# Performance work log

Measured on AMD Instinct MI355X. Metric: run time of the kernel, lower is better.

The kernel has to match this reference:

```python
import jax, jax.numpy as jnp
import numpy as np

N_NODES, N_EDGES, D, H = 100000, 640000, 128, 128


def setup_inputs() -> dict:
    key = jax.random.key(0)
    k = jax.random.split(key, 5)
    x = jax.random.normal(k[0], (N_NODES, D), dtype=jnp.float32)
    edge_idx = jax.random.randint(k[1], (2, N_EDGES), 0, N_NODES)
    eps = jnp.zeros((1,), dtype=jnp.float32)  # nn.Parameter(torch.zeros(1))
    # MLP params: Linear(D,H) -> ReLU -> Linear(H,D)
    W1 = jax.random.normal(k[2], (D, H), dtype=jnp.float32) / np.sqrt(D).astype(np.float32)
    b1 = jnp.zeros((H,), dtype=jnp.float32)
    W2 = jax.random.normal(k[3], (H, D), dtype=jnp.float32) / np.sqrt(H).astype(np.float32)
    b2 = jnp.zeros((D,), dtype=jnp.float32)
    return dict(x=x, edge_idx=edge_idx, eps=eps, W1=W1, b1=b1, W2=W2, b2=b2)


def reference(x, edge_idx, eps, W1, b1, W2, b2):
    # gather src node features, scatter-add into dst rows
    src, dst = edge_idx[0], edge_idx[1]
    agg = jax.ops.segment_sum(x[src], dst, num_segments=x.shape[0])  # [N, D]
    out = (1.0 + eps) * x + agg  # eps-weighted residual
    h = jax.nn.relu(out @ W1 + b1)
    return h @ W2 + b2
```

## Files before the change

kernel.cpp:

```cpp
#include <hip/hip_runtime.h>

#define DD 128
typedef unsigned int uint;
typedef unsigned short ushort;

typedef __attribute__((ext_vector_type(8))) __bf16 bf16x8;
typedef __attribute__((ext_vector_type(8))) short short8;
typedef __attribute__((ext_vector_type(4))) float f32x4;

__device__ inline short f2bf_bits(float f) {
  union { float f; unsigned u; } x; x.f = f;
  unsigned r = x.u + 0x7fffu + ((x.u >> 16) & 1u);
  return (short)(r >> 16);
}
__device__ inline float bflo(uint u) { return __uint_as_float(u << 16); }
__device__ inline float bfhi(uint u) { return __uint_as_float(u & 0xffff0000u); }

__global__ void k_zero(int* __restrict__ p, int n) {
  int i = blockIdx.x * blockDim.x + threadIdx.x;
  if (i < n) p[i] = 0;
}

#define CHUNK 2048
__global__ __launch_bounds__(256) void k_bin(const int* __restrict__ ei, int ne,
                                             int* __restrict__ scur, uint* __restrict__ pairs32,
                                             const float4* __restrict__ xf4,
                                             short8* __restrict__ xb8, int nx8,
                                             const float* __restrict__ W1,
                                             const float* __restrict__ W2,
                                             ushort* __restrict__ wbf, int nbins) {
  __shared__ uint st[CHUNK];
  __shared__ ushort stb[CHUNK];
  __shared__ int hist[512];
  __shared__ int sc[512];
  __shared__ int loff[512];
  __shared__ int cur[512];
  __shared__ int gb[512];

  const int tid = threadIdx.x;
  const int sb = blockIdx.x & 63;
  const long base = (long)blockIdx.x * CHUNK;
  int m = (int)(ne - base);
  if (m > CHUNK) m = CHUNK;
  if (m < 0) m = 0;

  const int i0 = tid, i1 = tid + 256;
  hist[i0] = 0; hist[i1] = 0;
  cur[i0] = 0;  cur[i1] = 0;
  __syncthreads();

  uint wreg[8];
  int breg[8];
#pragma unroll
  for (int i = 0; i < 8; ++i) {
    int idx = i * 256 + tid;
    if (idx < m) {
      uint s = (uint)ei[base + idx];
      uint d = (uint)ei[(long)ne + base + idx];
      breg[i] = (int)(d >> 8);
      wreg[i] = (s << 8) | (d & 255u);
      atomicAdd(&hist[breg[i]], 1);
    } else {
      breg[i] = -1;
    }
  }
  __syncthreads();

  sc[i0] = hist[i0]; sc[i1] = hist[i1];
  __syncthreads();
  for (int d = 1; d < 512; d <<= 1) {
    int t0 = (i0 >= d) ? sc[i0 - d] : 0;
    int t1 = (i1 >= d) ? sc[i1 - d] : 0;
    __syncthreads();
    sc[i0] += t0; sc[i1] += t1;
    __syncthreads();
  }
  loff[i0] = sc[i0] - hist[i0];
  loff[i1] = sc[i1] - hist[i1];
  if (i0 < nbins && hist[i0] > 0) gb[i0] = atomicAdd(&scur[i0 * 64 + sb], hist[i0]);
  if (i1 < nbins && hist[i1] > 0) gb[i1] = atomicAdd(&scur[i1 * 64 + sb], hist[i1]);
  __syncthreads();

#pragma unroll
  for (int i = 0; i < 8; ++i) {
    if (breg[i] >= 0) {
      int p = atomicAdd(&cur[breg[i]], 1);
      int pos = loff[breg[i]] + p;
      st[pos] = wreg[i];
      stb[pos] = (ushort)breg[i];
    }
  }
  __syncthreads();

  for (int i = tid; i < m; i += 256) {
    int b = stb[i];
    int k = i - loff[b];
    int g = gb[b] + k;
    if (g < 128)
      pairs32[(long)b * 16384 + (sb << 8) + g] = st[i];
  }

  int t = blockIdx.x * 256 + tid;
  int stride = gridDim.x * 256;
  for (int c = t; c < nx8; c += stride) {
    float4 a = xf4[2 * c], b = xf4[2 * c + 1];
    short8 o;
    o[0] = f2bf_bits(a.x); o[1] = f2bf_bits(a.y); o[2] = f2bf_bits(a.z); o[3] = f2bf_bits(a.w);
    o[4] = f2bf_bits(b.x); o[5] = f2bf_bits(b.y); o[6] = f2bf_bits(b.z); o[7] = f2bf_bits(b.w);
    xb8[c] = o;
  }
  if (t < 16384) {
    int k = t >> 7, n = t & 127;
    wbf[128 * n + 8 * ((k >> 3) ^ (n & 7)) + (k & 7)] = (ushort)f2bf_bits(W1[t]);
  } else if (t < 32768) {
    int e = t - 16384;
    int k = e >> 7, n = e & 127;
    wbf[16384 + 128 * n + 8 * ((k >> 3) ^ (n & 7)) + (k & 7)] = (ushort)f2bf_bits(W2[e]);
  }
}

#define SUBCAP 128
__global__ __launch_bounds__(256) void k_bucket(const uint* __restrict__ pairs32,
                                                const int* __restrict__ scur,
                                                int* __restrict__ slot,
                                                int* __restrict__ cnt, int n) {
  __shared__ uint st[64 * SUBCAP];
  __shared__ int cs[64];
  __shared__ int cur[256];
  const int b = blockIdx.x;
  const int tid = threadIdx.x;
  if (tid < 64) {
    int c = scur[b * 64 + tid];
    cs[tid] = c < SUBCAP ? c : SUBCAP;
  }
  cur[tid] = 0;
  __syncthreads();
  for (int k = tid; k < 64 * SUBCAP; k += 256) {
    int s = k >> 7, i = k & (SUBCAP - 1);
    if (i < cs[s]) st[k] = pairs32[(long)b * 16384 + (s << 8) + i];
  }
  __syncthreads();
  for (int k = tid; k < 64 * SUBCAP; k += 256) {
    int s = k >> 7, i = k & (SUBCAP - 1);
    if (i < cs[s]) {
      uint w = st[k];
      int d = (int)(w & 255u);
      int p = atomicAdd(&cur[d], 1);
      if (p < 64) slot[(long)b * 16384 + d * 64 + p] = (int)(w >> 8);
    }
  }
  __syncthreads();
  int node = (b << 8) + tid;
  if (node < n) cnt[node] = cur[tid];
}

__global__ __launch_bounds__(256) void k_agg2(const uint* __restrict__ xb,
                                              const float* __restrict__ eps,
                                              const int* __restrict__ cnt,
                                              const int* __restrict__ slot,
                                              uint* __restrict__ agb, int n) {
  int wv = (blockIdx.x * 256 + threadIdx.x) >> 6;
  int lane = threadIdx.x & 63;
  int r0 = wv * 2, r1 = r0 + 1;
  if (r0 >= n) return;
  bool has1 = (r1 < n);
  float s = 1.0f + eps[0];

  uint u0 = xb[(long)r0 * 64 + lane];
  float a0x = s * bflo(u0), a0y = s * bfhi(u0);
  int d0 = cnt[r0];
  int m0 = d0 < 64 ? d0 : 64;
  int src0 = (lane < m0) ? slot[(long)r0 * 64 + lane] : 0;

  float a1x = 0.0f, a1y = 0.0f;
  int m1 = 0, src1 = 0;
  if (has1) {
    uint u1 = xb[(long)r1 * 64 + lane];
    a1x = s * bflo(u1); a1y = s * bfhi(u1);
    int d1 = cnt[r1];
    m1 = d1 < 64 ? d1 : 64;
    src1 = (lane < m1) ? slot[(long)r1 * 64 + lane] : 0;
  }

  int mm = m0 > m1 ? m0 : m1;
  for (int j = 0; j < mm; j += 4) {
    uint v0[4], v1[4];
#pragma unroll
    for (int k = 0; k < 4; ++k) {
      if (j + k < m0) { int ss = __shfl(src0, j + k); v0[k] = xb[(long)ss * 64 + lane]; }
      if (j + k < m1) { int ss = __shfl(src1, j + k); v1[k] = xb[(long)ss * 64 + lane]; }
    }
#pragma unroll
    for (int k = 0; k < 4; ++k) {
      if (j + k < m0) { a0x += bflo(v0[k]); a0y += bfhi(v0[k]); }
      if (j + k < m1) { a1x += bflo(v1[k]); a1y += bfhi(v1[k]); }
    }
  }

  uint o0 = ((uint)(ushort)f2bf_bits(a0y) << 16) | (uint)(ushort)f2bf_bits(a0x);
  agb[(long)r0 * 64 + lane] = o0;
  if (has1) {
    uint o1 = ((uint)(ushort)f2bf_bits(a1y) << 16) | (uint)(ushort)f2bf_bits(a1x);
    agb[(long)r1 * 64 + lane] = o1;
  }
}

__global__ __launch_bounds__(256) void k_mlp_bf(const ushort* __restrict__ agb,
                                                const ushort* __restrict__ wbf,
                                                const float* __restrict__ b1,
                                                const float* __restrict__ b2,
                                                float* __restrict__ out, int nrows) {
  __shared__ __align__(16) short Wt[2 * 16384];
  __shared__ __align__(16) short Hb[4][16 * 128];

  const int tid = threadIdx.x;
  const int lane = tid & 63;
  const int w = tid >> 6;
  const int l15 = lane & 15;
  const int g = lane >> 4;
  const int brow = blockIdx.x * 128;

  {
    const short8* ws8 = (const short8*)wbf;
    short8* wd8 = (short8*)Wt;
#pragma unroll
    for (int it = 0; it < 16; ++it) wd8[it * 256 + tid] = ws8[it * 256 + tid];
  }

  union U8 { short8 s; bf16x8 b; };

  U8 afr[2][4];
#pragma unroll
  for (int h = 0; h < 2; ++h) {
    int arow = brow + 64 * h + 16 * w + l15;
    if (arow < nrows) {
      const short8* ap = reinterpret_cast<const short8*>(agb + (long)arow * DD);
#pragma unroll
      for (int s = 0; s < 4; ++s) afr[h][s].s = ap[4 * s + g];
    } else {
#pragma unroll
      for (int s = 0; s < 4; ++s) {
        short8 t;
#pragma unroll
        for (int jj = 0; jj < 8; ++jj) t[jj] = 0;
        afr[h][s].s = t;
      }
    }
  }

  __syncthreads();

#pragma unroll
  for (int h = 0; h < 2; ++h) {
    const int wrow = brow + 64 * h + 16 * w;

    f32x4 acc[8];
#pragma unroll
    for (int nf = 0; nf < 8; ++nf) acc[nf] = (f32x4)(0.0f);
#pragma unroll
    for (int s = 0; s < 4; ++s) {
#pragma unroll
      for (int nf = 0; nf < 8; ++nf) {
        int n = 16 * nf + l15;
        U8 bf;
        bf.s = *reinterpret_cast<const short8*>(&Wt[128 * n + 8 * (((s << 2) | g) ^ (n & 7))]);
        acc[nf] = __builtin_amdgcn_mfma_f32_16x16x32_bf16(afr[h][s].b, bf.b, acc[nf], 0, 0, 0);
      }
    }

#pragma unroll
    for (int nf = 0; nf < 8; ++nf) {
      int col = 16 * nf + l15;
      float bb = b1[col];
#pragma unroll
      for (int i = 0; i < 4; ++i) {
        int hrow = 4 * g + i;
        float v = acc[nf][i] + bb;
        v = fmaxf(v, 0.0f);
        Hb[w][128 * hrow + 8 * ((col >> 3) ^ (hrow & 7)) + (col & 7)] = f2bf_bits(v);
      }
    }

    U8 hfr[4];
#pragma unroll
    for (int s = 0; s < 4; ++s) {
      hfr[s].s = *reinterpret_cast<const short8*>(
          &Hb[w][128 * l15 + 8 * (((s << 2) | g) ^ (l15 & 7))]);
    }

    f32x4 acc2[8];
#pragma unroll
    for (int nf = 0; nf < 8; ++nf) acc2[nf] = (f32x4)(0.0f);
#pragma unroll
    for (int s = 0; s < 4; ++s) {
#pragma unroll
      for (int nf = 0; nf < 8; ++nf) {
        int n = 16 * nf + l15;
        U8 bf;
        bf.s = *reinterpret_cast<const short8*>(
            &Wt[16384 + 128 * n + 8 * (((s << 2) | g) ^ (n & 7))]);
        acc2[nf] = __builtin_amdgcn_mfma_f32_16x16x32_bf16(hfr[s].b, bf.b, acc2[nf], 0, 0, 0);
      }
    }

#pragma unroll
    for (int nf = 0; nf < 8; ++nf) {
      int col = 16 * nf + l15;
      float bb = b2[col];
#pragma unroll
      for (int i = 0; i < 4; ++i) {
        int grow = wrow + 4 * g + i;
        if (grow < nrows) out[(long)grow * DD + col] = acc2[nf][i] + bb;
      }
    }
  }
}

extern "C" void kernel_launch(void* const* d_in, const int* in_sizes, int n_in,
                              void* d_out, int out_size, void* d_ws, size_t ws_size,
                              hipStream_t stream) {
  const float* x   = (const float*)d_in[0];
  const int*   ei  = (const int*)d_in[1];
  const float* eps = (const float*)d_in[2];
  const float* W1  = (const float*)d_in[3];
  const float* b1  = (const float*)d_in[4];
  const float* W2  = (const float*)d_in[5];
  const float* b2  = (const float*)d_in[6];
  float* out = (float*)d_out;

  const int N  = in_sizes[0] / DD;
  const int NE = in_sizes[1] / 2;
  const int NBINS = (N + 255) >> 8;

  ushort* wbf = (ushort*)d_ws;
  ushort* xbf = wbf + 32768;
  uint* region = (uint*)(xbf + (size_t)N * DD);
  int* slot = (int*)region;
  uint* agb = region;
  int* scur = (int*)(region + (size_t)NBINS * 16384);
  int* cnt = scur + (size_t)NBINS * 64;

  int nz = NBINS * 64;
  k_zero<<<(nz + 255) / 256, 256, 0, stream>>>(scur, nz);

  int nblk = (NE + CHUNK - 1) / CHUNK;
  k_bin<<<nblk, 256, 0, stream>>>(
      ei, NE, scur, region, (const float4*)x, (short8*)xbf, N * (DD / 8),
      W1, W2, wbf, NBINS);

  k_bucket<<<NBINS, 256, 0, stream>>>(region, scur, slot, cnt, N);

  int nwv = (N + 1) / 2;
  k_agg2<<<(nwv * 64 + 255) / 256, 256, 0, stream>>>(
      (const uint*)xbf, eps, cnt, slot, agb, N);

  k_mlp_bf<<<(N + 127) / 128, 256, 0, stream>>>(
      (const ushort*)agb, wbf, b1, b2, out, N);
}
```

Before: 115.0 us.

## Move x and weight bf16 conversion into zero and bucket kernels

```diff
diff --git a/kernel.cpp b/kernel.cpp
--- a/kernel.cpp
+++ b/kernel.cpp
@@ -16,19 +16,25 @@
 __device__ inline float bflo(uint u) { return __uint_as_float(u << 16); }
 __device__ inline float bfhi(uint u) { return __uint_as_float(u & 0xffff0000u); }
 
-__global__ void k_zero(int* __restrict__ p, int n) {
+__global__ void k_zero_conv(int* __restrict__ p, int n,
+                            const float* __restrict__ W1, const float* __restrict__ W2,
+                            ushort* __restrict__ wbf) {
   int i = blockIdx.x * blockDim.x + threadIdx.x;
   if (i < n) p[i] = 0;
+  if (i < 16384) {
+    int k = i >> 7, nn = i & 127;
+    wbf[128 * nn + 8 * ((k >> 3) ^ (nn & 7)) + (k & 7)] = (ushort)f2bf_bits(W1[i]);
+  } else if (i < 32768) {
+    int e = i - 16384;
+    int k = e >> 7, nn = e & 127;
+    wbf[16384 + 128 * nn + 8 * ((k >> 3) ^ (nn & 7)) + (k & 7)] = (ushort)f2bf_bits(W2[e]);
+  }
 }
 
 #define CHUNK 2048
 __global__ __launch_bounds__(256) void k_bin(const int* __restrict__ ei, int ne,
                                              int* __restrict__ scur, uint* __restrict__ pairs32,
-                                             const float4* __restrict__ xf4,
-                                             short8* __restrict__ xb8, int nx8,
-                                             const float* __restrict__ W1,
-                                             const float* __restrict__ W2,
-                                             ushort* __restrict__ wbf, int nbins) {
+                                             int nbins) {
   __shared__ uint st[CHUNK];
   __shared__ ushort stb[CHUNK];
   __shared__ int hist[512];
@@ -99,36 +105,34 @@
     if (g < 128)
       pairs32[(long)b * 16384 + (sb << 8) + g] = st[i];
   }
-
-  int t = blockIdx.x * 256 + tid;
-  int stride = gridDim.x * 256;
-  for (int c = t; c < nx8; c += stride) {
-    float4 a = xf4[2 * c], b = xf4[2 * c + 1];
-    short8 o;
-    o[0] = f2bf_bits(a.x); o[1] = f2bf_bits(a.y); o[2] = f2bf_bits(a.z); o[3] = f2bf_bits(a.w);
-    o[4] = f2bf_bits(b.x); o[5] = f2bf_bits(b.y); o[6] = f2bf_bits(b.z); o[7] = f2bf_bits(b.w);
-    xb8[c] = o;
-  }
-  if (t < 16384) {
-    int k = t >> 7, n = t & 127;
-    wbf[128 * n + 8 * ((k >> 3) ^ (n & 7)) + (k & 7)] = (ushort)f2bf_bits(W1[t]);
-  } else if (t < 32768) {
-    int e = t - 16384;
-    int k = e >> 7, n = e & 127;
-    wbf[16384 + 128 * n + 8 * ((k >> 3) ^ (n & 7)) + (k & 7)] = (ushort)f2bf_bits(W2[e]);
-  }
 }
 
 #define SUBCAP 128
-__global__ __launch_bounds__(256) void k_bucket(const uint* __restrict__ pairs32,
-                                                const int* __restrict__ scur,
-                                                int* __restrict__ slot,
-                                                int* __restrict__ cnt, int n) {
+__global__ __launch_bounds__(256) void k_bucket_conv(const uint* __restrict__ pairs32,
+                                                     const int* __restrict__ scur,
+                                                     int* __restrict__ slot,
+                                                     int* __restrict__ cnt, int n, int nbins,
+                                                     const float4* __restrict__ xf4,
+                                                     short8* __restrict__ xb8, int nx8) {
   __shared__ uint st[64 * SUBCAP];
   __shared__ int cs[64];
   __shared__ int cur[256];
   const int b = blockIdx.x;
   const int tid = threadIdx.x;
+
+  if (b >= nbins) {
+    int cb = b - nbins;
+    int stride = (gridDim.x - nbins) * 256;
+    for (int c = cb * 256 + tid; c < nx8; c += stride) {
+      float4 a = xf4[2 * c], bb = xf4[2 * c + 1];
+      short8 o;
+      o[0] = f2bf_bits(a.x); o[1] = f2bf_bits(a.y); o[2] = f2bf_bits(a.z); o[3] = f2bf_bits(a.w);
+      o[4] = f2bf_bits(bb.x); o[5] = f2bf_bits(bb.y); o[6] = f2bf_bits(bb.z); o[7] = f2bf_bits(bb.w);
+      xb8[c] = o;
+    }
+    return;
+  }
+
   if (tid < 64) {
     int c = scur[b * 64 + tid];
     cs[tid] = c < SUBCAP ? c : SUBCAP;
@@ -341,14 +345,14 @@
   int* cnt = scur + (size_t)NBINS * 64;
 
   int nz = NBINS * 64;
-  k_zero<<<(nz + 255) / 256, 256, 0, stream>>>(scur, nz);
+  k_zero_conv<<<128, 256, 0, stream>>>(scur, nz, W1, W2, wbf);
 
   int nblk = (NE + CHUNK - 1) / CHUNK;
-  k_bin<<<nblk, 256, 0, stream>>>(
-      ei, NE, scur, region, (const float4*)x, (short8*)xbf, N * (DD / 8),
-      W1, W2, wbf, NBINS);
-
-  k_bucket<<<NBINS, 256, 0, stream>>>(region, scur, slot, cnt, N);
+  k_bin<<<nblk, 256, 0, stream>>>(ei, NE, scur, region, NBINS);
+
+  const int NCONVB = 1024;
+  k_bucket_conv<<<NBINS + NCONVB, 256, 0, stream>>>(
+      region, scur, slot, cnt, N, NBINS, (const float4*)x, (short8*)xbf, N * (DD / 8));
 
   int nwv = (N + 1) / 2;
   k_agg2<<<(nwv * 64 + 255) / 256, 256, 0, stream>>>(
```

After: 110.3 us. 4.1% less time.
